# Optimization experiments

Hardware: AMD Instinct MI355X
Metric: run time of the kernel (lower is better)

Reference implementation:

```python
import jax, jax.numpy as jnp
import numpy as np

B, T, D, E, F = 4, 2048, 1024, 8, 1024

def setup_inputs() -> dict:
    key = jax.random.key(0)
    ks = jax.random.split(key, 5)
    s = lambda d: 1.0 / np.sqrt(d)
    return {
        "x": jax.random.normal(ks[0], (B, T, D), dtype=jnp.float32),
        "router_kernel_DE": jax.random.normal(ks[1], (D, E), dtype=jnp.float32) * s(D),
        "kernel_gating_EDF": jax.random.normal(ks[2], (E, D, F), dtype=jnp.float32) * s(D),
        "kernel_up_EDF": jax.random.normal(ks[3], (E, D, F), dtype=jnp.float32) * s(D),
        "kernel_down_EFD": jax.random.normal(ks[4], (E, F, D), dtype=jnp.float32) * s(F),
        "top_k": 2,
    }

def reference(x, router_kernel_DE, kernel_gating_EDF, kernel_up_EDF, kernel_down_EFD, top_k):
    # ---- Router ----
    router_logits_BTE = jnp.einsum('BTD,DE->BTE', x, router_kernel_DE)
    probs_BTE = jax.nn.softmax(router_logits_BTE.astype(jnp.float32), axis=-1)
    weights_BTX, selected_BTX = jax.lax.top_k(probs_BTE, top_k)
    # module re-normalizes top-k weights with a second softmax (faithful)
    norm_weights_BTX = jax.nn.softmax(weights_BTX, axis=-1)
    # ---- combine weights to dense per-expert weights ----
    one_hot_BTXE = jax.nn.one_hot(selected_BTX, num_classes=E, dtype=jnp.float32)
    full_weights_BTE = jnp.sum(one_hot_BTXE * norm_weights_BTX[..., None], axis=2)
    # ---- dense all-experts MLP (apply_expert_weight_before_computation=False) ----
    gating_BTEF = jnp.einsum('BTD,EDF->BTEF', x, kernel_gating_EDF)
    up_BTEF = jnp.einsum('BTD,EDF->BTEF', x, kernel_up_EDF)
    fuse_BTEF = jax.nn.silu(gating_BTEF) * up_BTEF
    down_BTED = jnp.einsum('BTEF,EFD->BTED', fuse_BTEF, kernel_down_EFD)
    out_BTD = jnp.einsum('BTED,BTE->BTD', down_BTED, full_weights_BTE)
    return out_BTD
```

## Files before the change

kernel.cpp:

```cpp
#include <hip/hip_runtime.h>
#include <hip/hip_bf16.h>
#include <math.h>

#define NTOK 8192
#define D_DIM 1024
#define E_DIM 8
#define F_DIM 1024

#define CNT_STRIDE 32

typedef __attribute__((ext_vector_type(8))) short bf16x8;
typedef __attribute__((ext_vector_type(4))) float f32x4;

typedef const __attribute__((address_space(1))) unsigned int* as1_uint_ptr;
typedef __attribute__((address_space(3))) unsigned int* as3_uint_ptr;

__device__ __forceinline__ void async_load16(const void* g, void* l) {
    __builtin_amdgcn_global_load_lds((as1_uint_ptr)g, (as3_uint_ptr)l, 16, 0, 0);
}

__device__ __forceinline__ float bf2f(unsigned short b) {
    unsigned int u = ((unsigned int)b) << 16;
    return __builtin_bit_cast(float, u);
}
__device__ __forceinline__ unsigned short f2bf(float f) {
    __hip_bfloat16 h = __float2bfloat16(f);
    return __builtin_bit_cast(unsigned short, h);
}


__global__ __launch_bounds__(512) void router_cast_kernel(
    const float* __restrict__ x,
    const float* __restrict__ Wr,
    int* __restrict__ cnt,
    int* __restrict__ tok_of,
    float* __restrict__ wt2,
    unsigned short* __restrict__ xb)
{
    __shared__ int lcnt[E_DIM];
    __shared__ int lbase[E_DIM];
    __shared__ int lbuf[E_DIM][64];

    const int tid = threadIdx.x;
    const int wv = tid >> 6;
    const int lane = tid & 63;
    if (tid < E_DIM) lcnt[tid] = 0;
    __syncthreads();

    #pragma unroll
    for (int it = 0; it < 4; ++it) {
        const int t = blockIdx.x * 32 + wv * 4 + it;
        const float* xrow = x + (size_t)t * D_DIM;
        unsigned short* xbrow = xb + (size_t)t * D_DIM;

        float p[E_DIM];
        #pragma unroll
        for (int e = 0; e < E_DIM; ++e) p[e] = 0.f;

        #pragma unroll
        for (int i = 0; i < 4; ++i) {
            const int d = i * 256 + lane * 4;
            float4 v = *(const float4*)(xrow + d);
            ushort4 o;
            o.x = f2bf(v.x); o.y = f2bf(v.y); o.z = f2bf(v.z); o.w = f2bf(v.w);
            *(ushort4*)(xbrow + d) = o;
            const float* wr = Wr + (size_t)d * E_DIM;
            float xv[4] = {v.x, v.y, v.z, v.w};
            #pragma unroll
            for (int q = 0; q < 4; ++q) {
                float4 w0 = *(const float4*)(wr + q * 8);
                float4 w1 = *(const float4*)(wr + q * 8 + 4);
                p[0] += xv[q] * w0.x; p[1] += xv[q] * w0.y;
                p[2] += xv[q] * w0.z; p[3] += xv[q] * w0.w;
                p[4] += xv[q] * w1.x; p[5] += xv[q] * w1.y;
                p[6] += xv[q] * w1.z; p[7] += xv[q] * w1.w;
            }
        }

        #pragma unroll
        for (int off = 32; off > 0; off >>= 1) {
            #pragma unroll
            for (int e = 0; e < E_DIM; ++e)
                p[e] += __shfl_xor(p[e], off, 64);
        }

        if (lane == 0) {
            float m = p[0];
            #pragma unroll
            for (int e = 1; e < E_DIM; ++e) m = fmaxf(m, p[e]);
            float pr[E_DIM], sum = 0.f;
            #pragma unroll
            for (int e = 0; e < E_DIM; ++e) { pr[e] = expf(p[e] - m); sum += pr[e]; }
            float inv = 1.f / sum;
            #pragma unroll
            for (int e = 0; e < E_DIM; ++e) pr[e] *= inv;
            int e0 = 0;
            #pragma unroll
            for (int e = 1; e < E_DIM; ++e) if (pr[e] > pr[e0]) e0 = e;
            int e1 = (e0 == 0) ? 1 : 0;
            #pragma unroll
            for (int e = 0; e < E_DIM; ++e) { if (e != e0 && pr[e] > pr[e1]) e1 = e; }
            float b = expf(pr[e1] - pr[e0]);
            float w0 = 1.f / (1.f + b);
            float w1 = b / (1.f + b);
            int p0 = atomicAdd(&lcnt[e0], 1);
            lbuf[e0][p0] = t * 2 + 0;
            int p1 = atomicAdd(&lcnt[e1], 1);
            lbuf[e1][p1] = t * 2 + 1;
            wt2[t * 2 + 0] = w0;
            wt2[t * 2 + 1] = w1;
        }
    }
    __syncthreads();
    if (tid < E_DIM) lbase[tid] = atomicAdd(&cnt[tid * CNT_STRIDE], lcnt[tid]);
    __syncthreads();
    #pragma unroll
    for (int e = 0; e < E_DIM; ++e) {
        int n = lcnt[e];
        if (tid < n) tok_of[e * NTOK + lbase[e] + tid] = lbuf[e][tid];
    }
}

__global__ __launch_bounds__(256) void transpose_cast_kernel(
    const float* __restrict__ Wg, const float* __restrict__ Wu,
    const float* __restrict__ Wd,
    unsigned short* __restrict__ WgT, unsigned short* __restrict__ WuT,
    unsigned short* __restrict__ WdT)
{
    const int m = blockIdx.z;
    const float* src;
    unsigned short* dst;
    if (m < 8)       { src = Wg + (size_t)m * 1048576;        dst = WgT + (size_t)m * 1048576; }
    else if (m < 16) { src = Wu + (size_t)(m - 8) * 1048576;  dst = WuT + (size_t)(m - 8) * 1048576; }
    else             { src = Wd + (size_t)(m - 16) * 1048576; dst = WdT + (size_t)(m - 16) * 1048576; }

    const int c0 = blockIdx.x * 64;
    const int r0 = blockIdx.y * 64;
    __shared__ float tile[64][65];
    const int tid = threadIdx.x;
    const int tr = tid >> 4;
    const int tc = (tid & 15) * 4;
    #pragma unroll
    for (int p = 0; p < 4; ++p) {
        float4 v = *(const float4*)(src + (size_t)(r0 + p * 16 + tr) * 1024 + c0 + tc);
        tile[p * 16 + tr][tc + 0] = v.x;
        tile[p * 16 + tr][tc + 1] = v.y;
        tile[p * 16 + tr][tc + 2] = v.z;
        tile[p * 16 + tr][tc + 3] = v.w;
    }
    __syncthreads();
    const int orow = tid >> 3;
    const int ocol = (tid & 7) * 8;
    #pragma unroll
    for (int p = 0; p < 2; ++p) {
        int fr = p * 32 + orow;
        union { unsigned short s[8]; uint4 v; } pk;
        #pragma unroll
        for (int q = 0; q < 8; ++q) pk.s[q] = f2bf(tile[ocol + q][fr]);
        *(uint4*)&dst[(size_t)(c0 + fr) * 1024 + r0 + ocol] = pk.v;
    }
}

__global__ __launch_bounds__(256, 2) void gateup_mfma(
    const unsigned short* __restrict__ xb,
    const unsigned short* __restrict__ WgT,
    const unsigned short* __restrict__ WuT,
    const int* __restrict__ cnt,
    const int* __restrict__ tok_of,
    unsigned short* __restrict__ H)
{
    const int colTile = blockIdx.x & 7;
    const int wk = blockIdx.x >> 3;
    int e = -1, rowBase = 0, rows = 0, tb = 0;
    #pragma unroll
    for (int q = 0; q < E_DIM; ++q) {
        int r = cnt[q * CNT_STRIDE];
        int nt = (r + 127) >> 7;
        if (e < 0 && wk < tb + nt) { e = q; rowBase = (wk - tb) << 7; rows = r; }
        tb += nt;
    }
    if (e < 0) return;
    const int n0 = colTile * 128;

    __shared__ short As[2][128 * 32];
    __shared__ short Bg[2][128 * 32];
    __shared__ short Bu[2][128 * 32];
    __shared__ int toks[128];

    const int tid = threadIdx.x;
    if (tid < 128) {
        int idx = rowBase + tid;
        toks[tid] = tok_of[e * NTOK + (idx < rows ? idx : rows - 1)];
    }
    __syncthreads();

    const int lane = tid & 63;
    const int w = tid >> 6;
    const int seg0 = w * 2, seg1 = w * 2 + 1;
    const int sr = lane >> 2;
    const int swz = (sr >> 1) & 3;
    const int sk = ((lane & 3) ^ swz) * 8;

    const int ar0 = seg0 * 16 + sr;
    const int ar1 = seg1 * 16 + sr;
    const unsigned short* aG0 = xb + (size_t)(toks[ar0] >> 1) * D_DIM + sk;
    const unsigned short* aG1 = xb + (size_t)(toks[ar1] >> 1) * D_DIM + sk;
    const unsigned short* WgTe = WgT + (size_t)e * F_DIM * D_DIM;
    const unsigned short* WuTe = WuT + (size_t)e * F_DIM * D_DIM;
    const unsigned short* gG0 = WgTe + (size_t)(n0 + ar0) * D_DIM + sk;
    const unsigned short* gG1 = WgTe + (size_t)(n0 + ar1) * D_DIM + sk;
    const unsigned short* uG0 = WuTe + (size_t)(n0 + ar0) * D_DIM + sk;
    const unsigned short* uG1 = WuTe + (size_t)(n0 + ar1) * D_DIM + sk;

    const int mseg = (w >> 1) * 4;
    const int nseg = (w & 1) * 4;
    const int mbase = (w >> 1) * 64;
    const int nbase = (w & 1) * 64;
    const int fr = lane & 15;
    const int rd = (4 * fr + ((lane >> 4) ^ ((fr >> 1) & 3))) * 8;

    f32x4 accg[4][4], accu[4][4];
    #pragma unroll
    for (int i = 0; i < 4; ++i)
        #pragma unroll
        for (int j = 0; j < 4; ++j) { accg[i][j] = (f32x4)(0.f); accu[i][j] = (f32x4)(0.f); }

    #define STAGE_GU(b, kk) do { \
        async_load16(aG0 + (kk), &As[b][seg0 * 512]); \
        async_load16(aG1 + (kk), &As[b][seg1 * 512]); \
        async_load16(gG0 + (kk), &Bg[b][seg0 * 512]); \
        async_load16(gG1 + (kk), &Bg[b][seg1 * 512]); \
        async_load16(uG0 + (kk), &Bu[b][seg0 * 512]); \
        async_load16(uG1 + (kk), &Bu[b][seg1 * 512]); \
    } while (0)

    const int NT = D_DIM / 32;
    STAGE_GU(0, 0);
    STAGE_GU(1, 32);

    #pragma unroll 2
    for (int t = 0; t < NT - 1; ++t) {
        const int b = t & 1;
        asm volatile("s_waitcnt vmcnt(6)" ::: "memory");
        __builtin_amdgcn_s_barrier();

        bf16x8 a[4], g[4], u[4];
        #pragma unroll
        for (int i = 0; i < 4; ++i)
            a[i] = *(const bf16x8*)&As[b][(mseg + i) * 512 + rd];
        #pragma unroll
        for (int j = 0; j < 4; ++j) {
            g[j] = *(const bf16x8*)&Bg[b][(nseg + j) * 512 + rd];
            u[j] = *(const bf16x8*)&Bu[b][(nseg + j) * 512 + rd];
        }
        asm volatile("s_waitcnt lgkmcnt(0)" ::: "memory");
        __builtin_amdgcn_sched_barrier(0);
        __builtin_amdgcn_s_barrier();
        if (t < NT - 2) STAGE_GU(b, (t + 2) * 32);

        __builtin_amdgcn_s_setprio(1);
        #pragma unroll
        for (int i = 0; i < 4; ++i)
            #pragma unroll
            for (int j = 0; j < 4; ++j) {
                accg[i][j] = __builtin_amdgcn_mfma_f32_16x16x32_bf16(a[i], g[j], accg[i][j], 0, 0, 0);
                accu[i][j] = __builtin_amdgcn_mfma_f32_16x16x32_bf16(a[i], u[j], accu[i][j], 0, 0, 0);
            }
        __builtin_amdgcn_s_setprio(0);
    }
    {
        asm volatile("s_waitcnt vmcnt(0)" ::: "memory");
        __builtin_amdgcn_s_barrier();
        bf16x8 a[4], g[4], u[4];
        #pragma unroll
        for (int i = 0; i < 4; ++i)
            a[i] = *(const bf16x8*)&As[1][(mseg + i) * 512 + rd];
        #pragma unroll
        for (int j = 0; j < 4; ++j) {
            g[j] = *(const bf16x8*)&Bg[1][(nseg + j) * 512 + rd];
            u[j] = *(const bf16x8*)&Bu[1][(nseg + j) * 512 + rd];
        }
        __builtin_amdgcn_s_setprio(1);
        #pragma unroll
        for (int i = 0; i < 4; ++i)
            #pragma unroll
            for (int j = 0; j < 4; ++j) {
                accg[i][j] = __builtin_amdgcn_mfma_f32_16x16x32_bf16(a[i], g[j], accg[i][j], 0, 0, 0);
                accu[i][j] = __builtin_amdgcn_mfma_f32_16x16x32_bf16(a[i], u[j], accu[i][j], 0, 0, 0);
            }
        __builtin_amdgcn_s_setprio(0);
    }
    #undef STAGE_GU

    const int erow = (lane >> 4) * 4;
    #pragma unroll
    for (int i = 0; i < 4; ++i) {
        #pragma unroll
        for (int r = 0; r < 4; ++r) {
            int row = mbase + i * 16 + erow + r;
            int idx = rowBase + row;
            if (idx < rows) {
                int tok2 = toks[row];
                unsigned short* hrow = H + (size_t)tok2 * F_DIM + n0 + nbase;
                #pragma unroll
                for (int j = 0; j < 4; ++j) {
                    float gg = accg[i][j][r];
                    float uu = accu[i][j][r];
                    float h = gg / (1.f + __expf(-gg)) * uu;
                    hrow[j * 16 + fr] = f2bf(h);
                }
            }
        }
    }
}

__global__ __launch_bounds__(256, 2) void down_mfma(
    const unsigned short* __restrict__ H,
    const unsigned short* __restrict__ WdT,
    const int* __restrict__ cnt,
    const int* __restrict__ tok_of,
    unsigned short* __restrict__ Hd)
{
    const int colTile = blockIdx.x & 7;
    const int wk = blockIdx.x >> 3;
    int e = -1, rowBase = 0, rows = 0, tb = 0;
    #pragma unroll
    for (int q = 0; q < E_DIM; ++q) {
        int r = cnt[q * CNT_STRIDE];
        int nt = (r + 127) >> 7;
        if (e < 0 && wk < tb + nt) { e = q; rowBase = (wk - tb) << 7; rows = r; }
        tb += nt;
    }
    if (e < 0) return;
    const int n0 = colTile * 128;

    __shared__ short As[2][128 * 32];
    __shared__ short Bs[2][128 * 32];
    __shared__ int toks[128];

    const int tid = threadIdx.x;
    if (tid < 128) {
        int idx = rowBase + tid;
        toks[tid] = tok_of[e * NTOK + (idx < rows ? idx : rows - 1)];
    }
    __syncthreads();

    const int lane = tid & 63;
    const int w = tid >> 6;
    const int seg0 = w * 2, seg1 = w * 2 + 1;
    const int sr = lane >> 2;
    const int swz = (sr >> 1) & 3;
    const int sk = ((lane & 3) ^ swz) * 8;

    const int ar0 = seg0 * 16 + sr;
    const int ar1 = seg1 * 16 + sr;
    const unsigned short* aG0 = H + (size_t)toks[ar0] * F_DIM + sk;
    const unsigned short* aG1 = H + (size_t)toks[ar1] * F_DIM + sk;
    const unsigned short* WdTe = WdT + (size_t)e * D_DIM * F_DIM;
    const unsigned short* bG0 = WdTe + (size_t)(n0 + ar0) * F_DIM + sk;
    const unsigned short* bG1 = WdTe + (size_t)(n0 + ar1) * F_DIM + sk;

    const int mseg = (w >> 1) * 4;
    const int nseg = (w & 1) * 4;
    const int mbase = (w >> 1) * 64;
    const int nbase = (w & 1) * 64;
    const int fr = lane & 15;
    const int rd = (4 * fr + ((lane >> 4) ^ ((fr >> 1) & 3))) * 8;

    f32x4 acc[4][4];
    #pragma unroll
    for (int i = 0; i < 4; ++i)
        #pragma unroll
        for (int j = 0; j < 4; ++j) acc[i][j] = (f32x4)(0.f);

    #define STAGE_D(b, kk) do { \
        async_load16(aG0 + (kk), &As[b][seg0 * 512]); \
        async_load16(aG1 + (kk), &As[b][seg1 * 512]); \
        async_load16(bG0 + (kk), &Bs[b][seg0 * 512]); \
        async_load16(bG1 + (kk), &Bs[b][seg1 * 512]); \
    } while (0)

    const int NT = F_DIM / 32;
    STAGE_D(0, 0);
    STAGE_D(1, 32);

    #pragma unroll 2
    for (int t = 0; t < NT - 1; ++t) {
        const int b = t & 1;
        asm volatile("s_waitcnt vmcnt(4)" ::: "memory");
        __builtin_amdgcn_s_barrier();

        bf16x8 a[4], bb[4];
        #pragma unroll
        for (int i = 0; i < 4; ++i)
            a[i] = *(const bf16x8*)&As[b][(mseg + i) * 512 + rd];
        #pragma unroll
        for (int j = 0; j < 4; ++j)
            bb[j] = *(const bf16x8*)&Bs[b][(nseg + j) * 512 + rd];

        asm volatile("s_waitcnt lgkmcnt(0)" ::: "memory");
        __builtin_amdgcn_sched_barrier(0);
        __builtin_amdgcn_s_barrier();
        if (t < NT - 2) STAGE_D(b, (t + 2) * 32);

        __builtin_amdgcn_s_setprio(1);
        #pragma unroll
        for (int i = 0; i < 4; ++i)
            #pragma unroll
            for (int j = 0; j < 4; ++j)
                acc[i][j] = __builtin_amdgcn_mfma_f32_16x16x32_bf16(a[i], bb[j], acc[i][j], 0, 0, 0);
        __builtin_amdgcn_s_setprio(0);
    }
    {
        asm volatile("s_waitcnt vmcnt(0)" ::: "memory");
        __builtin_amdgcn_s_barrier();
        bf16x8 a[4], bb[4];
        #pragma unroll
        for (int i = 0; i < 4; ++i)
            a[i] = *(const bf16x8*)&As[1][(mseg + i) * 512 + rd];
        #pragma unroll
        for (int j = 0; j < 4; ++j)
            bb[j] = *(const bf16x8*)&Bs[1][(nseg + j) * 512 + rd];
        __builtin_amdgcn_s_setprio(1);
        #pragma unroll
        for (int i = 0; i < 4; ++i)
            #pragma unroll
            for (int j = 0; j < 4; ++j)
                acc[i][j] = __builtin_amdgcn_mfma_f32_16x16x32_bf16(a[i], bb[j], acc[i][j], 0, 0, 0);
        __builtin_amdgcn_s_setprio(0);
    }
    #undef STAGE_D

    const int erow = (lane >> 4) * 4;
    #pragma unroll
    for (int i = 0; i < 4; ++i) {
        #pragma unroll
        for (int r = 0; r < 4; ++r) {
            int row = mbase + i * 16 + erow + r;
            int idx = rowBase + row;
            if (idx < rows) {
                int tok2 = toks[row];
                unsigned short* orow = Hd + (size_t)tok2 * D_DIM + n0 + nbase;
                #pragma unroll
                for (int j = 0; j < 4; ++j)
                    orow[j * 16 + fr] = f2bf(acc[i][j][r]);
            }
        }
    }
}

__global__ __launch_bounds__(256) void combine_kernel(
    const unsigned short* __restrict__ Hd,
    const float* __restrict__ wt2,
    float* __restrict__ out)
{
    const int t = blockIdx.x;
    const int tid = threadIdx.x;
    const float w0 = wt2[2 * t];
    const float w1 = wt2[2 * t + 1];
    const int c = tid * 4;
    ushort4 a = *(const ushort4*)&Hd[(size_t)(2 * t) * D_DIM + c];
    ushort4 b = *(const ushort4*)&Hd[(size_t)(2 * t + 1) * D_DIM + c];
    float4 o;
    o.x = w0 * bf2f(a.x) + w1 * bf2f(b.x);
    o.y = w0 * bf2f(a.y) + w1 * bf2f(b.y);
    o.z = w0 * bf2f(a.z) + w1 * bf2f(b.z);
    o.w = w0 * bf2f(a.w) + w1 * bf2f(b.w);
    *(float4*)(out + (size_t)t * D_DIM + c) = o;
}

extern "C" void kernel_launch(void* const* d_in, const int* in_sizes, int n_in,
                              void* d_out, int out_size, void* d_ws, size_t ws_size,
                              hipStream_t stream) {
    const float* x  = (const float*)d_in[0];
    const float* Wr = (const float*)d_in[1];
    const float* Wg = (const float*)d_in[2];
    const float* Wu = (const float*)d_in[3];
    const float* Wd = (const float*)d_in[4];
    float* out = (float*)d_out;

    char* ws = (char*)d_ws;
    int*   cnt    = (int*)ws;
    int*   tok_of = (int*)(ws + 1024);
    float* wt2    = (float*)(ws + 1024 + E_DIM * NTOK * 4);
    char*  base   = ws + (1 << 20);
    unsigned short* xb  = (unsigned short*)(base);
    unsigned short* Hd  = (unsigned short*)(base);
    unsigned short* WgT = (unsigned short*)(base + (16ll << 20));
    unsigned short* WuT = (unsigned short*)(base + (32ll << 20));
    unsigned short* WdT = (unsigned short*)(base + (48ll << 20));
    unsigned short* H   = (unsigned short*)(base + (64ll << 20));

    hipMemsetAsync(cnt, 0, E_DIM * CNT_STRIDE * sizeof(int), stream);

    router_cast_kernel<<<NTOK / 32, 512, 0, stream>>>(x, Wr, cnt, tok_of, wt2, xb);
    transpose_cast_kernel<<<dim3(16, 16, 24), 256, 0, stream>>>(Wg, Wu, Wd, WgT, WuT, WdT);

    const int MAX_TILES = (2 * NTOK) / 128 + E_DIM;
    gateup_mfma<<<dim3(MAX_TILES * 8), 256, 0, stream>>>(
        xb, WgT, WuT, cnt, tok_of, H);
    down_mfma<<<dim3(MAX_TILES * 8), 256, 0, stream>>>(
        H, WdT, cnt, tok_of, Hd);
    combine_kernel<<<NTOK, 256, 0, stream>>>(Hd, wt2, out);
}
```

Baseline: 359.2 us.

## Merge router and weight transpose kernels; fuse combine into down GEMM via atomics

Router/cast and weight transpose-cast run as one launch: blocks 0-255 do routing, the rest each handle two 64x64 transpose tiles. The separate combine kernel is removed. The down GEMM now scales its output by the routing weight and atomically adds fp32 values into a zeroed output buffer, so the bf16 Hd intermediate write and re-read disappear. The cost is an extra output memset, fp32 atomics at scalar granularity, and a summation order that is no longer deterministic.

New measurement: 376.6 us. 1.05x slower.

```diff
diff --git a/kernel.cpp b/kernel.cpp
--- a/kernel.cpp
+++ b/kernel.cpp
@@ -29,19 +29,63 @@
 }
 
 
-__global__ __launch_bounds__(512) void router_cast_kernel(
+__global__ __launch_bounds__(512) void prep_kernel(
     const float* __restrict__ x,
     const float* __restrict__ Wr,
     int* __restrict__ cnt,
     int* __restrict__ tok_of,
     float* __restrict__ wt2,
-    unsigned short* __restrict__ xb)
+    unsigned short* __restrict__ xb,
+    const float* __restrict__ Wg, const float* __restrict__ Wu,
+    const float* __restrict__ Wd,
+    unsigned short* __restrict__ WgT, unsigned short* __restrict__ WuT,
+    unsigned short* __restrict__ WdT)
 {
+    const int tid = threadIdx.x;
+
+    if (blockIdx.x >= 256) {
+        __shared__ float tile[2][64][65];
+        const int s = tid >> 8;
+        const int t2 = tid & 255;
+        const int k = (blockIdx.x - 256) * 2 + s;
+        const int m = k >> 8;
+        const int rem = k & 255;
+        const int c0 = (rem & 15) * 64;
+        const int r0 = (rem >> 4) * 64;
+        const float* src;
+        unsigned short* dst;
+        if (m < 8)       { src = Wg + (size_t)m * 1048576;        dst = WgT + (size_t)m * 1048576; }
+        else if (m < 16) { src = Wu + (size_t)(m - 8) * 1048576;  dst = WuT + (size_t)(m - 8) * 1048576; }
+        else             { src = Wd + (size_t)(m - 16) * 1048576; dst = WdT + (size_t)(m - 16) * 1048576; }
+
+        const int tr = t2 >> 4;
+        const int tc = (t2 & 15) * 4;
+        #pragma unroll
+        for (int p = 0; p < 4; ++p) {
+            float4 v = *(const float4*)(src + (size_t)(r0 + p * 16 + tr) * 1024 + c0 + tc);
+            tile[s][p * 16 + tr][tc + 0] = v.x;
+            tile[s][p * 16 + tr][tc + 1] = v.y;
+            tile[s][p * 16 + tr][tc + 2] = v.z;
+            tile[s][p * 16 + tr][tc + 3] = v.w;
+        }
+        __syncthreads();
+        const int orow = t2 >> 3;
+        const int ocol = (t2 & 7) * 8;
+        #pragma unroll
+        for (int p = 0; p < 2; ++p) {
+            int fr = p * 32 + orow;
+            union { unsigned short us[8]; uint4 v; } pk;
+            #pragma unroll
+            for (int q = 0; q < 8; ++q) pk.us[q] = f2bf(tile[s][ocol + q][fr]);
+            *(uint4*)&dst[(size_t)(c0 + fr) * 1024 + r0 + ocol] = pk.v;
+        }
+        return;
+    }
+
     __shared__ int lcnt[E_DIM];
     __shared__ int lbase[E_DIM];
     __shared__ int lbuf[E_DIM][64];
 
-    const int tid = threadIdx.x;
     const int wv = tid >> 6;
     const int lane = tid & 63;
     if (tid < E_DIM) lcnt[tid] = 0;
@@ -118,46 +162,6 @@
     for (int e = 0; e < E_DIM; ++e) {
         int n = lcnt[e];
         if (tid < n) tok_of[e * NTOK + lbase[e] + tid] = lbuf[e][tid];
-    }
-}
-
-__global__ __launch_bounds__(256) void transpose_cast_kernel(
-    const float* __restrict__ Wg, const float* __restrict__ Wu,
-    const float* __restrict__ Wd,
-    unsigned short* __restrict__ WgT, unsigned short* __restrict__ WuT,
-    unsigned short* __restrict__ WdT)
-{
-    const int m = blockIdx.z;
-    const float* src;
-    unsigned short* dst;
-    if (m < 8)       { src = Wg + (size_t)m * 1048576;        dst = WgT + (size_t)m * 1048576; }
-    else if (m < 16) { src = Wu + (size_t)(m - 8) * 1048576;  dst = WuT + (size_t)(m - 8) * 1048576; }
-    else             { src = Wd + (size_t)(m - 16) * 1048576; dst = WdT + (size_t)(m - 16) * 1048576; }
-
-    const int c0 = blockIdx.x * 64;
-    const int r0 = blockIdx.y * 64;
-    __shared__ float tile[64][65];
-    const int tid = threadIdx.x;
-    const int tr = tid >> 4;
-    const int tc = (tid & 15) * 4;
-    #pragma unroll
-    for (int p = 0; p < 4; ++p) {
-        float4 v = *(const float4*)(src + (size_t)(r0 + p * 16 + tr) * 1024 + c0 + tc);
-        tile[p * 16 + tr][tc + 0] = v.x;
-        tile[p * 16 + tr][tc + 1] = v.y;
-        tile[p * 16 + tr][tc + 2] = v.z;
-        tile[p * 16 + tr][tc + 3] = v.w;
-    }
-    __syncthreads();
-    const int orow = tid >> 3;
-    const int ocol = (tid & 7) * 8;
-    #pragma unroll
-    for (int p = 0; p < 2; ++p) {
-        int fr = p * 32 + orow;
-        union { unsigned short s[8]; uint4 v; } pk;
-        #pragma unroll
-        for (int q = 0; q < 8; ++q) pk.s[q] = f2bf(tile[ocol + q][fr]);
-        *(uint4*)&dst[(size_t)(c0 + fr) * 1024 + r0 + ocol] = pk.v;
     }
 }
 
@@ -319,7 +323,8 @@
     const unsigned short* __restrict__ WdT,
     const int* __restrict__ cnt,
     const int* __restrict__ tok_of,
-    unsigned short* __restrict__ Hd)
+    const float* __restrict__ wt2,
+    float* __restrict__ out)
 {
     const int colTile = blockIdx.x & 7;
     const int wk = blockIdx.x >> 3;
@@ -440,33 +445,14 @@
             int idx = rowBase + row;
             if (idx < rows) {
                 int tok2 = toks[row];
-                unsigned short* orow = Hd + (size_t)tok2 * D_DIM + n0 + nbase;
+                float wgt = wt2[tok2];
+                float* orow = out + (size_t)(tok2 >> 1) * D_DIM + n0 + nbase;
                 #pragma unroll
                 for (int j = 0; j < 4; ++j)
-                    orow[j * 16 + fr] = f2bf(acc[i][j][r]);
+                    atomicAdd(&orow[j * 16 + fr], acc[i][j][r] * wgt);
             }
         }
     }
-}
-
-__global__ __launch_bounds__(256) void combine_kernel(
-    const unsigned short* __restrict__ Hd,
-    const float* __restrict__ wt2,
-    float* __restrict__ out)
-{
-    const int t = blockIdx.x;
-    const int tid = threadIdx.x;
-    const float w0 = wt2[2 * t];
-    const float w1 = wt2[2 * t + 1];
-    const int c = tid * 4;
-    ushort4 a = *(const ushort4*)&Hd[(size_t)(2 * t) * D_DIM + c];
-    ushort4 b = *(const ushort4*)&Hd[(size_t)(2 * t + 1) * D_DIM + c];
-    float4 o;
-    o.x = w0 * bf2f(a.x) + w1 * bf2f(b.x);
-    o.y = w0 * bf2f(a.y) + w1 * bf2f(b.y);
-    o.z = w0 * bf2f(a.z) + w1 * bf2f(b.z);
-    o.w = w0 * bf2f(a.w) + w1 * bf2f(b.w);
-    *(float4*)(out + (size_t)t * D_DIM + c) = o;
 }
 
 extern "C" void kernel_launch(void* const* d_in, const int* in_sizes, int n_in,
@@ -485,21 +471,20 @@
     float* wt2    = (float*)(ws + 1024 + E_DIM * NTOK * 4);
     char*  base   = ws + (1 << 20);
     unsigned short* xb  = (unsigned short*)(base);
-    unsigned short* Hd  = (unsigned short*)(base);
     unsigned short* WgT = (unsigned short*)(base + (16ll << 20));
     unsigned short* WuT = (unsigned short*)(base + (32ll << 20));
     unsigned short* WdT = (unsigned short*)(base + (48ll << 20));
     unsigned short* H   = (unsigned short*)(base + (64ll << 20));
 
     hipMemsetAsync(cnt, 0, E_DIM * CNT_STRIDE * sizeof(int), stream);
-
-    router_cast_kernel<<<NTOK / 32, 512, 0, stream>>>(x, Wr, cnt, tok_of, wt2, xb);
-    transpose_cast_kernel<<<dim3(16, 16, 24), 256, 0, stream>>>(Wg, Wu, Wd, WgT, WuT, WdT);
+    hipMemsetAsync(out, 0, (size_t)NTOK * D_DIM * sizeof(float), stream);
+
+    prep_kernel<<<256 + 3072, 512, 0, stream>>>(
+        x, Wr, cnt, tok_of, wt2, xb, Wg, Wu, Wd, WgT, WuT, WdT);
 
     const int MAX_TILES = (2 * NTOK) / 128 + E_DIM;
     gateup_mfma<<<dim3(MAX_TILES * 8), 256, 0, stream>>>(
         xb, WgT, WuT, cnt, tok_of, H);
     down_mfma<<<dim3(MAX_TILES * 8), 256, 0, stream>>>(
-        H, WdT, cnt, tok_of, Hd);
-    combine_kernel<<<NTOK, 256, 0, stream>>>(Hd, wt2, out);
-}
+        H, WdT, cnt, tok_of, wt2, out);
+}
```
